# Optimization experiments

Measured on AMD Instinct MI355X. Metric: run time of the kernel, lower is better.

Reference implementation:

```python
import jax, jax.numpy as jnp
import numpy as np

B, N, D = 64, 256, 64          # datasets, samples per dataset, feature dim per variable (indim/2)
H, H2, OUT = 128, 64, 3        # hdlayers, hdlayers//2, outdim
REG, SIGMA, ALPHA = 1.0, 1.0, 2
BN_EPS = 1e-5


def _linear(k, fan_in, fan_out):
    kw, kb = jax.random.split(k)
    lim = 1.0 / np.sqrt(fan_in)
    w = jax.random.uniform(kw, (fan_in, fan_out), jnp.float32, -lim, lim)
    b = jax.random.uniform(kb, (fan_out,), jnp.float32, -lim, lim)
    return w, b


def setup_inputs() -> dict:
    key = jax.random.key(0)
    ks = jax.random.split(key, 10)
    w11_1, b11_1 = _linear(ks[2], D, H2)
    w11_2, b11_2 = _linear(ks[3], H2, H2)
    w12_1, b12_1 = _linear(ks[4], 2 * H2, H)
    w12_2, b12_2 = _linear(ks[5], H, H2)
    wc1, bc1 = _linear(ks[6], H2, OUT)
    w2, b2 = _linear(ks[7], OUT + 2, H2)
    wc2, bc2 = _linear(ks[8], H2, OUT)
    return {
        'x': jax.random.normal(ks[0], (B, N, D), jnp.float32),
        'y': jax.random.normal(ks[1], (B, N, D), jnp.float32),
        'w11_1': w11_1, 'b11_1': b11_1, 'w11_2': w11_2, 'b11_2': b11_2,
        'w12_1': w12_1, 'b12_1': b12_1, 'w12_2': w12_2, 'b12_2': b12_2,
        'wc1': wc1, 'bc1': bc1,
        'bn_gamma': jnp.ones((OUT + 2,), jnp.float32),
        'bn_beta': jnp.zeros((OUT + 2,), jnp.float32),
        'w2': w2, 'b2': b2, 'wc2': wc2, 'bc2': bc2,
    }


def _fro_normalize(t):
    # divide each [N, D] slice by its Frobenius norm
    return t / jnp.linalg.norm(t, axis=(1, 2), keepdims=True)


def _linear_regressor(x, y, reg):
    b, n, d = x.shape
    X = jnp.concatenate([jnp.ones((b, n, 1), x.dtype), x], axis=2)  # [B,N,d+1]
    P1 = jnp.einsum('bni,bnj->bij', X, X)                           # X^T X
    ridge = reg * jnp.eye(d + 1, dtype=x.dtype).at[0, 0].set(0.0)   # G^T G
    P2 = jnp.linalg.inv(P1 + ridge[None])
    P4 = X @ (P2 @ (jnp.swapaxes(X, 1, 2) @ y))
    loss = jnp.sum((y - P4) ** 2, axis=(1, 2))
    return loss, P4


def _gauss_kernel(x):
    # x: [B, N, F] -> [B, N, N]
    xn = jnp.sum(x * x, axis=-1)
    dist = xn[:, :, None] + xn[:, None, :] - 2.0 * jnp.einsum('bnd,bmd->bnm', x, x)
    return jnp.exp(-dist / SIGMA)


def _renyi_from_kernel(k):
    tr = jnp.trace(k, axis1=1, axis2=2)
    k = k / tr[:, None, None]
    ev = jnp.abs(jnp.linalg.eigvalsh(k))          # batched symeig eigenvalues
    return (1.0 / (1 - ALPHA)) * jnp.log2(jnp.sum(ev ** ALPHA, axis=-1))


def _renyi_mi(a, b):
    # batched normalized Renyi mutual information, a/b: [B, N, F]
    ka, kb = _gauss_kernel(a), _gauss_kernel(b)
    Hx = _renyi_from_kernel(ka)
    Hy = _renyi_from_kernel(kb)
    Hxy = _renyi_from_kernel(ka * kb)
    return (Hx + Hy - Hxy) / jnp.maximum(Hx, Hy)


def reference(x, y, w11_1, b11_1, w11_2, b11_2, w12_1, b12_1, w12_2, b12_2,
              wc1, bc1, bn_gamma, bn_beta, w2, b2, wc2, bc2):
    mlp11 = lambda t: jnp.maximum(t @ w11_1 + b11_1, 0.0) @ w11_2 + b11_2
    out_x = mlp11(x)                                  # [B,N,H2]
    out_y = mlp11(y)

    out_c = jnp.concatenate([out_x, out_y], axis=2)   # [B,N,2*H2]
    out_c = jnp.maximum(out_c @ w12_1 + b12_1, 0.0)
    out_c = jnp.maximum(out_c @ w12_2 + b12_2, 0.0)
    out_c = out_c.mean(axis=1)                        # [B,H2]
    out_c = out_c @ wc1 + bc1                         # [B,OUT]
    prob1 = jax.nn.softmax(out_c, axis=1)

    out_xn = _fro_normalize(out_x)
    out_yn = _fro_normalize(out_y)
    xx = _fro_normalize(x)
    yy = _fro_normalize(y)

    rx, px = _linear_regressor(out_xn, yy, REG)       # predict y from f(x)
    ry, py = _linear_regressor(out_yn, xx, REG)       # predict x from f(y)

    ex = _renyi_mi(yy - px, x)                        # [B]
    ey = _renyi_mi(xx - py, y)

    rxy = jnp.stack([ex, ey], axis=1)                 # [B,2]
    in_c = jnp.concatenate([out_c, rxy], axis=1)      # [B,OUT+2]
    mu = in_c.mean(axis=0)
    var = in_c.var(axis=0)                            # biased, as in torch BN training
    in_c = (in_c - mu) / jnp.sqrt(var + BN_EPS) * bn_gamma + bn_beta
    in_c = jnp.maximum(in_c @ w2 + b2, 0.0)
    out_c_f = in_c @ wc2 + bc2
    prob2 = jax.nn.softmax(out_c_f, axis=1)

    return (out_c, rx, ry, ex, ey, out_c_f, prob1, prob2)
```

## Files before the change

### kernel.cpp

```cpp
#include <hip/hip_runtime.h>
#include <math.h>

#define NB 64
#define NS 256
#define ND 64
#define NH2 64
#define NH 128
#define GSTRIDE 8448
#define WSTRIDE 4224


#define F4E(v_, e_) ((e_)==0?(v_).x:((e_)==1?(v_).y:((e_)==2?(v_).z:(v_).w)))

typedef __attribute__((ext_vector_type(8))) short bf16x8;
typedef __attribute__((ext_vector_type(4))) float f32x4;

__device__ __forceinline__ unsigned short f2bf(float f){
    union { float f; unsigned int u; } v; v.f = f;
    unsigned int r = v.u + 0x7fffu + ((v.u >> 16) & 1u);
    return (unsigned short)(r >> 16);
}
__device__ __forceinline__ float bf2f(unsigned short h){
    union { unsigned int u; float f; } v; v.u = ((unsigned int)h) << 16;
    return v.f;
}
__device__ __forceinline__ void sw2(unsigned short* ph, unsigned short* pl, int idx, float f){
    unsigned short h = f2bf(f);
    ph[idx] = h;
    pl[idx] = f2bf(f - bf2f(h));
}
__device__ __forceinline__ void sw2x2(unsigned short* ph, unsigned short* pl, int idx, float f0, float f1){
    unsigned short h0 = f2bf(f0), h1 = f2bf(f1);
    ushort2 hh; hh.x = h0; hh.y = h1;
    *(ushort2*)(ph + idx) = hh;
    ushort2 ll; ll.x = f2bf(f0 - bf2f(h0)); ll.y = f2bf(f1 - bf2f(h1));
    *(ushort2*)(pl + idx) = ll;
}

#define LD8(P_, row_, kb_) (*(const bf16x8*)((const char*)(P_) + (size_t)(row_)*144 + (kb_)))

__device__ __forceinline__ f32x4 mm64(
    const unsigned short* Ah, const unsigned short* Al,
    const unsigned short* Bh, const unsigned short* Bl,
    int ar, int br, int lrow, int lkb, f32x4 acc)
{
    const int ra = ar + lrow, rb = br + lrow;
    bf16x8 ah0 = LD8(Ah, ra, lkb), ah1 = LD8(Ah, ra, lkb+64);
    bf16x8 al0 = LD8(Al, ra, lkb), al1 = LD8(Al, ra, lkb+64);
    bf16x8 bh0 = LD8(Bh, rb, lkb), bh1 = LD8(Bh, rb, lkb+64);
    bf16x8 bl0 = LD8(Bl, rb, lkb), bl1 = LD8(Bl, rb, lkb+64);
    acc = __builtin_amdgcn_mfma_f32_16x16x32_bf16(ah0, bh0, acc, 0,0,0);
    acc = __builtin_amdgcn_mfma_f32_16x16x32_bf16(ah1, bh1, acc, 0,0,0);
    acc = __builtin_amdgcn_mfma_f32_16x16x32_bf16(ah0, bl0, acc, 0,0,0);
    acc = __builtin_amdgcn_mfma_f32_16x16x32_bf16(ah1, bl1, acc, 0,0,0);
    acc = __builtin_amdgcn_mfma_f32_16x16x32_bf16(al0, bh0, acc, 0,0,0);
    acc = __builtin_amdgcn_mfma_f32_16x16x32_bf16(al1, bh1, acc, 0,0,0);
    return acc;
}

__global__ __launch_bounds__(256) void k1_fused(
    const float* __restrict__ x, const float* __restrict__ y,
    const float* __restrict__ w11_1, const float* __restrict__ b11_1,
    const float* __restrict__ w11_2, const float* __restrict__ b11_2,
    const float* __restrict__ w12_1, const float* __restrict__ b12_1,
    const float* __restrict__ w12_2, const float* __restrict__ b12_2,
    float* __restrict__ out_x, float* __restrict__ out_y,
    float* __restrict__ mean_part)
{
    const int b = blockIdx.x >> 2, tile = blockIdx.x & 3;
    const int t = threadIdx.x;
    const int lane = t & 63, wv = t >> 6;
    const int lrow = lane & 15;
    const int lkb  = (lane >> 4) * 16;
    const int row0g = b*NS + tile*64;

    __shared__ unsigned short XYh[9216], XYl[9216];
    __shared__ unsigned short W1h[4608], W1l[4608];
    __shared__ unsigned short W2h[4608], W2l[4608];
    __shared__ unsigned short Hh [9216], Hl [9216];
    __shared__ unsigned short Oh [9216], Ol [9216];
    __shared__ float msum[4*68];

    #pragma unroll
    for (int u=0;u<8;u++){
        int id = t + 256*u;
        int r = id>>4, c0 = (id&15)*4;
        const float* src = (r < 64) ? (x + ((size_t)(row0g + r))*ND)
                                    : (y + ((size_t)(row0g + r - 64))*ND);
        float4 v = *(const float4*)(src + c0);
        sw2x2(XYh, XYl, r*72 + c0,   v.x, v.y);
        sw2x2(XYh, XYl, r*72 + c0+2, v.z, v.w);
    }
    #pragma unroll
    for (int u=0;u<2;u++){
        int id = t + 256*u;
        int rp = id>>4, c0 = (id&15)*4;
        float4 a0 = *(const float4*)(w11_1 + (size_t)(2*rp  )*64 + c0);
        float4 a1 = *(const float4*)(w11_1 + (size_t)(2*rp+1)*64 + c0);
        float4 b0 = *(const float4*)(w11_2 + (size_t)(2*rp  )*64 + c0);
        float4 b1 = *(const float4*)(w11_2 + (size_t)(2*rp+1)*64 + c0);
        #pragma unroll
        for (int i2=0;i2<4;i2++){
            sw2x2(W1h, W1l, (c0+i2)*72 + 2*rp, F4E(a0,i2), F4E(a1,i2));
            sw2x2(W2h, W2l, (c0+i2)*72 + 2*rp, F4E(b0,i2), F4E(b1,i2));
        }
    }
    __syncthreads();

    #pragma unroll
    for (int it=0; it<2; it++){
        const int ar = 32*wv + 16*it;
        #pragma unroll
        for (int jt=0; jt<4; jt++){
            float bb = b11_1[jt*16 + lrow];
            f32x4 acc = {bb,bb,bb,bb};
            acc = mm64(XYh, XYl, W1h, W1l, ar, jt*16, lrow, lkb, acc);
            #pragma unroll
            for (int e=0;e<4;e++){
                int row = ar + (lane>>4)*4 + e;
                int col = jt*16 + lrow;
                sw2(Hh, Hl, row*72 + col, fmaxf(acc[e], 0.f));
            }
        }
    }
    __syncthreads();

    #pragma unroll
    for (int u=0;u<4;u++){
        int id = t + 256*u;
        int krp = id>>5, c0 = (id&31)*4;
        float4 v0 = *(const float4*)(w12_1 + (size_t)(2*krp  )*NH + c0);
        float4 v1 = *(const float4*)(w12_1 + (size_t)(2*krp+1)*NH + c0);
        #pragma unroll
        for (int i2=0;i2<4;i2++)
            sw2x2(XYh, XYl, (c0+i2)*72 + 2*krp, F4E(v0,i2), F4E(v1,i2));
    }
    #pragma unroll
    for (int it=0; it<2; it++){
        const int ar = 32*wv + 16*it;
        #pragma unroll
        for (int jt=0; jt<4; jt++){
            float bb = b11_2[jt*16 + lrow];
            f32x4 acc = {bb,bb,bb,bb};
            acc = mm64(Hh, Hl, W2h, W2l, ar, jt*16, lrow, lkb, acc);
            #pragma unroll
            for (int e=0;e<4;e++){
                int row = ar + (lane>>4)*4 + e;
                int col = jt*16 + lrow;
                float v = acc[e];
                sw2(Oh, Ol, row*72 + col, v);
                float* dst = (row < 64) ? out_x : out_y;
                dst[((size_t)(row0g + (row & 63)))*NH2 + col] = v;
            }
        }
    }
    __syncthreads();

    f32x4 acc3[8];
    #pragma unroll
    for (int jt=0; jt<8; jt++){
        float bb = b12_1[jt*16 + lrow];
        f32x4 v = {bb,bb,bb,bb};
        acc3[jt] = v;
    }
    #pragma unroll
    for (int jt=0; jt<8; jt++)
        acc3[jt] = mm64(Oh, Ol, XYh, XYl, 16*wv, jt*16, lrow, lkb, acc3[jt]);
    __syncthreads();

    #pragma unroll
    for (int u=0;u<4;u++){
        int id = t + 256*u;
        int krp = id>>5, c0 = (id&31)*4;
        float4 v0 = *(const float4*)(w12_1 + (size_t)(64+2*krp  )*NH + c0);
        float4 v1 = *(const float4*)(w12_1 + (size_t)(64+2*krp+1)*NH + c0);
        #pragma unroll
        for (int i2=0;i2<4;i2++)
            sw2x2(XYh, XYl, (c0+i2)*72 + 2*krp, F4E(v0,i2), F4E(v1,i2));
    }
    #pragma unroll
    for (int u=0;u<2;u++){
        int id = t + 256*u;
        int krp = id>>4, c0 = (id&15)*4;
        float4 h0a = *(const float4*)(w12_2 + (size_t)(2*krp  )*NH2 + c0);
        float4 h0b = *(const float4*)(w12_2 + (size_t)(2*krp+1)*NH2 + c0);
        float4 h1a = *(const float4*)(w12_2 + (size_t)(64+2*krp  )*NH2 + c0);
        float4 h1b = *(const float4*)(w12_2 + (size_t)(64+2*krp+1)*NH2 + c0);
        #pragma unroll
        for (int i2=0;i2<4;i2++){
            sw2x2(W2h, W2l, (c0+i2)*72 + 2*krp, F4E(h0a,i2), F4E(h0b,i2));
            sw2x2(W1h, W1l, (c0+i2)*72 + 2*krp, F4E(h1a,i2), F4E(h1b,i2));
        }
    }
    __syncthreads();

    #pragma unroll
    for (int jt=0; jt<8; jt++)
        acc3[jt] = mm64(Oh, Ol, XYh, XYl, 64 + 16*wv, jt*16, lrow, lkb, acc3[jt]);
    #pragma unroll
    for (int jt=0; jt<8; jt++){
        #pragma unroll
        for (int e=0;e<4;e++){
            int row = 16*wv + (lane>>4)*4 + e;
            int col = jt*16 + lrow;
            float v = fmaxf(acc3[jt][e], 0.f);
            int idx = (col < 64) ? (row*72 + col) : ((64+row)*72 + (col-64));
            sw2(Hh, Hl, idx, v);
        }
    }
    __syncthreads();

    {
        f32x4 acc2[4];
        #pragma unroll
        for (int jt=0; jt<4; jt++){
            float bb = b12_2[jt*16 + lrow];
            f32x4 v = {bb,bb,bb,bb};
            acc2[jt] = v;
        }
        #pragma unroll
        for (int jt=0; jt<4; jt++){
            acc2[jt] = mm64(Hh, Hl, W2h, W2l, 16*wv,      jt*16, lrow, lkb, acc2[jt]);
            acc2[jt] = mm64(Hh, Hl, W1h, W1l, 64 + 16*wv, jt*16, lrow, lkb, acc2[jt]);
        }
        #pragma unroll
        for (int jt=0; jt<4; jt++){
            float s = fmaxf(acc2[jt][0],0.f) + fmaxf(acc2[jt][1],0.f)
                    + fmaxf(acc2[jt][2],0.f) + fmaxf(acc2[jt][3],0.f);
            s += __shfl_down(s, 32);
            s += __shfl_down(s, 16);
            if (lane < 16) msum[wv*68 + jt*16 + lane] = s;
        }
    }
    __syncthreads();
    if (t < 64){
        float ss = msum[t] + msum[68+t] + msum[2*68+t] + msum[3*68+t];
        mean_part[((size_t)(b*4+tile))*64 + t] = ss;
    }
}

__global__ __launch_bounds__(256) void k2a_build(
    const float* __restrict__ fx, const float* __restrict__ fy,
    const float* __restrict__ x, const float* __restrict__ y,
    float* __restrict__ gram)
{
    const int blk = blockIdx.x;
    const int kh = blk & 1, side = (blk>>1)&1, b = blk>>2;
    const float* feat = side ? fy : fx;
    const float* targ = side ? x : y;
    float* g = gram + (size_t)blk*GSTRIDE;
    const int t = threadIdx.x;
    const int ig2 = t & 15, jg2 = t >> 4;
    const int i0 = ig2*4, j0 = jg2*4;
    __shared__ float Zt[64*68], Tt[64*68];
    __shared__ float red[4];

    float accA[4][4], accR[4][4];
    #pragma unroll
    for (int u=0;u<4;u++)
        #pragma unroll
        for (int v=0;v<4;v++){ accA[u][v]=0.f; accR[u][v]=0.f; }
    float szp=0.f, stp=0.f, tsqp=0.f;
    const int cc_ = t & 63, rq = t >> 6;

    for (int sub=0; sub<2; sub++){
        if (sub) __syncthreads();
        const int r0g = b*NS + kh*128 + sub*64;
        #pragma unroll
        for (int u=0;u<4;u++){
            int id = t + 256*u; int r = id>>4, c4 = (id&15)*4;
            *(float4*)(Zt + r*68 + c4) = *(const float4*)(feat + ((size_t)(r0g+r))*NH2 + c4);
            *(float4*)(Tt + r*68 + c4) = *(const float4*)(targ + ((size_t)(r0g+r))*ND + c4);
        }
        __syncthreads();
        #pragma unroll
        for (int ch=0; ch<16; ch++){
            const int r0 = ch*4;
            float4 zi[4], zj[4], tj[4];
            #pragma unroll
            for (int c=0;c<4;c++){
                zi[c] = *(const float4*)(Zt + (r0+c)*68 + i0);
                zj[c] = *(const float4*)(Zt + (r0+c)*68 + j0);
                tj[c] = *(const float4*)(Tt + (r0+c)*68 + j0);
            }
            #pragma unroll
            for (int c=0;c<4;c++){
                #pragma unroll
                for (int u=0;u<4;u++){
                    const float zv = F4E(zi[c], u);
                    const float4 a4 = zj[c], r4 = tj[c];
                    accA[u][0] += zv*a4.x; accA[u][1] += zv*a4.y;
                    accA[u][2] += zv*a4.z; accA[u][3] += zv*a4.w;
                    accR[u][0] += zv*r4.x; accR[u][1] += zv*r4.y;
                    accR[u][2] += zv*r4.z; accR[u][3] += zv*r4.w;
                }
            }
        }
        #pragma unroll
        for (int rr=0; rr<16; rr++){
            int r = rq*16 + rr;
            szp += Zt[r*68 + cc_];
            float tv = Tt[r*68 + cc_];
            stp += tv; tsqp += tv*tv;
        }
    }
    #pragma unroll
    for (int u=0;u<4;u++){
        *(float4*)(g + (i0+u)*64 + j0) = make_float4(accA[u][0],accA[u][1],accA[u][2],accA[u][3]);
        *(float4*)(g + 4096 + (i0+u)*64 + j0) = make_float4(accR[u][0],accR[u][1],accR[u][2],accR[u][3]);
    }
    __syncthreads();
    Zt[rq*68 + cc_] = szp;
    Tt[rq*68 + cc_] = stp;
    float tq = tsqp;
    #pragma unroll
    for (int off=32; off; off>>=1) tq += __shfl_down(tq, off);
    if ((t&63)==0) red[t>>6] = tq;
    __syncthreads();
    if (t < 64){
        g[8192+t] = Zt[t] + Zt[68+t] + Zt[2*68+t] + Zt[3*68+t];
        g[8256+t] = Tt[t] + Tt[68+t] + Tt[2*68+t] + Tt[3*68+t];
    }
    if (t==0) g[8320] = red[0]+red[1]+red[2]+red[3];
}

__global__ __launch_bounds__(256) void k2b_solve(
    const float* __restrict__ gram, float* __restrict__ wbuf)
{
    const int bs = blockIdx.x;
    const float* g0 = gram + (size_t)(bs*2+0)*GSTRIDE;
    const float* g1 = gram + (size_t)(bs*2+1)*GSTRIDE;
    float* wb = wbuf + (size_t)bs*WSTRIDE;
    const int t = threadIdx.x;
    const int lane = t & 63, wv = t >> 6;
    const int lrow = lane & 15;
    const int lkb  = (lane >> 4) * 16;

    __shared__ float Rf[64*68];
    __shared__ float Wf[64*68];
    __shared__ unsigned short Eh[4608], El[4608];
    __shared__ unsigned short Wth[2][4608], Wtl[2][4608];
    __shared__ float szs[64], sts[64];
    __shared__ float sc[8];

    #pragma unroll
    for (int u=0;u<16;u++){
        int id = t + 256*u; int r = id>>6, c = id&63;
        Wf[r*68+c] = g0[id] + g1[id];
        Rf[r*68+c] = g0[4096+id] + g1[4096+id];
    }
    if (t<64){ szs[t] = g0[8192+t]+g1[8192+t]; sts[t] = g0[8256+t]+g1[8256+t]; }
    if (t==0) sc[1] = g0[8320]+g1[8320];
    __syncthreads();
    if (t<64){
        float dg = Wf[t*68+t];
        #pragma unroll
        for (int off=32; off; off>>=1) dg += __shfl_down(dg, off);
        if (t==0){ sc[0] = 1.0f/sqrtf(dg); sc[1] = 1.0f/sqrtf(sc[1]); }
    }
    __syncthreads();
    const float zinv = sc[0], tinv = sc[1];
    const float z2 = zinv*zinv, zt = zinv*tinv, inv256 = 1.0f/256.0f;
    const float i23 = 2.0f/3.0f;
    const int i = t>>2, qd = t&3;
    {
        const float szi = szs[i];
        #pragma unroll
        for (int q=0;q<4;q++){
            const int j = qd*16 + q*4;
            float4 a4 = *(const float4*)(Wf + i*68 + j);
            float4 sj = *(const float4*)(szs + j);
            float v0 = z2*(a4.x - szi*sj.x*inv256);
            float v1 = z2*(a4.y - szi*sj.y*inv256);
            float v2 = z2*(a4.z - szi*sj.z*inv256);
            float v3 = z2*(a4.w - szi*sj.w*inv256);
            if (i == j)   v0 += 1.f;
            else if (i == j+1) v1 += 1.f;
            else if (i == j+2) v2 += 1.f;
            else if (i == j+3) v3 += 1.f;
            float e0 = v0*i23 - ((i==j  ) ? 1.f : 0.f);
            float e1 = v1*i23 - ((i==j+1) ? 1.f : 0.f);
            float e2 = v2*i23 - ((i==j+2) ? 1.f : 0.f);
            float e3 = v3*i23 - ((i==j+3) ? 1.f : 0.f);
            sw2x2(Eh, El, i*72 + j,   e0, e1);
            sw2x2(Eh, El, i*72 + j+2, e2, e3);
            float4 rv = *(float4*)(Rf + i*68 + j);
            float4 t4 = *(const float4*)(sts + j);
            float r0 = zt*(rv.x - szi*t4.x*inv256)*i23;
            float r1 = zt*(rv.y - szi*t4.y*inv256)*i23;
            float r2 = zt*(rv.z - szi*t4.z*inv256)*i23;
            float r3 = zt*(rv.w - szi*t4.w*inv256)*i23;
            *(float4*)(Rf + i*68 + j) = make_float4(r0,r1,r2,r3);
            sw2(Wth[0], Wtl[0], (j  )*72 + i, r0);
            sw2(Wth[0], Wtl[0], (j+1)*72 + i, r1);
            sw2(Wth[0], Wtl[0], (j+2)*72 + i, r2);
            sw2(Wth[0], Wtl[0], (j+3)*72 + i, r3);
        }
    }
    __syncthreads();

    int cur = 0;
    for (int n=0; n<12; n++){
        f32x4 acc[4];
        #pragma unroll
        for (int jt=0; jt<4; jt++){
            f32x4 zz = {0.f,0.f,0.f,0.f};
            acc[jt] = mm64(Eh, El, Wth[cur], Wtl[cur], 16*wv, jt*16, lrow, lkb, zz);
        }
        const int gi0 = 16*wv + (lane>>4)*4;
        #pragma unroll
        for (int jt=0; jt<4; jt++){
            const int gj = jt*16 + lrow;
            float w0 = Rf[(gi0  )*68 + gj] - acc[jt][0];
            float w1 = Rf[(gi0+1)*68 + gj] - acc[jt][1];
            float w2 = Rf[(gi0+2)*68 + gj] - acc[jt][2];
            float w3 = Rf[(gi0+3)*68 + gj] - acc[jt][3];
            sw2x2(Wth[cur^1], Wtl[cur^1], gj*72 + gi0,   w0, w1);
            sw2x2(Wth[cur^1], Wtl[cur^1], gj*72 + gi0+2, w2, w3);
            if (n == 11){
                Wf[(gi0  )*68 + gj] = w0;  wb[(gi0  )*64 + gj] = w0;
                Wf[(gi0+1)*68 + gj] = w1;  wb[(gi0+1)*64 + gj] = w1;
                Wf[(gi0+2)*68 + gj] = w2;  wb[(gi0+2)*64 + gj] = w2;
                Wf[(gi0+3)*68 + gj] = w3;  wb[(gi0+3)*64 + gj] = w3;
            }
        }
        cur ^= 1;
        __syncthreads();
    }

    if (t < 64){
        float s = 0.f;
        for (int i2=0; i2<64; i2++) s += szs[i2]*Wf[i2*68 + t];
        wb[4096+t] = (tinv*sts[t] - zinv*s) * inv256;
    }
    if (t==0){ wb[4160] = zinv; wb[4161] = tinv; }
}

__global__ __launch_bounds__(256) void kRG(
    const float* __restrict__ fx, const float* __restrict__ fy,
    const float* __restrict__ x, const float* __restrict__ y,
    const float* __restrict__ wbuf,
    float* __restrict__ part3, float* __restrict__ dout)
{
    const int blk = blockIdx.x;
    const int jh = blk & 1;
    const int b = (blk >> 1) & (NB-1);
    const int side = (blk >> 1) >> 6;
    const float* feat = side ? fy : fx;
    const float* targ = side ? x : y;
    const float* bmat = side ? y : x;
    const float* wb = wbuf + (size_t)(b*2+side)*WSTRIDE;
    const int t = threadIdx.x;
    const int lane = t & 63, wv = t >> 6;
    const int lrow = lane & 15, lkb = (lane>>4)*16;

    __shared__ unsigned short resA[256*72];
    __shared__ unsigned short tgB [256*72];
    __shared__ unsigned short Zh[2*4608], Zl[2*4608];
    __shared__ unsigned short Wth[4608], Wtl[4608];
    __shared__ float c0s[64];
    __shared__ float nAs[256], nBs[256];
    __shared__ float red[4][3];
    __shared__ float lred[4];

    #pragma unroll
    for (int u=0;u<4;u++){
        int id = t + 256*u;
        int k = id>>4, c0 = (id&15)*4;
        float4 v = *(const float4*)(wb + (size_t)k*64 + c0);
        sw2(Wth, Wtl, (c0+0)*72 + k, v.x);
        sw2(Wth, Wtl, (c0+1)*72 + k, v.y);
        sw2(Wth, Wtl, (c0+2)*72 + k, v.z);
        sw2(Wth, Wtl, (c0+3)*72 + k, v.w);
    }
    if (t<64) c0s[t] = wb[4096+t];
    const float zinv = wb[4160], tinv = wb[4161];
    #pragma unroll
    for (int u=0;u<16;u++){
        int id = t + 256*u;
        int r = id>>4, c0 = (id&15)*4;
        float4 v = *(const float4*)(bmat + ((size_t)(b*NS+r))*ND + c0);
        ushort4 h;
        h.x=f2bf(v.x); h.y=f2bf(v.y); h.z=f2bf(v.z); h.w=f2bf(v.w);
        *(ushort4*)(tgB + r*72 + c0) = h;
    }
    #pragma unroll
    for (int u=0;u<4;u++){
        int id = t + 256*u;
        int r = id>>4, c0 = (id&15)*4;
        float4 v = *(const float4*)(feat + ((size_t)(b*NS + r))*NH2 + c0);
        sw2x2(Zh, Zl, r*72+c0,   v.x, v.y);
        sw2x2(Zh, Zl, r*72+c0+2, v.z, v.w);
    }
    __syncthreads();

    float lacc = 0.f;
    for (int c=0; c<4; c++){
        if (c < 3){
            unsigned short* zh = Zh + ((c+1)&1)*4608;
            unsigned short* zl = Zl + ((c+1)&1)*4608;
            #pragma unroll
            for (int u=0;u<4;u++){
                int id = t + 256*u;
                int r = id>>4, c0 = (id&15)*4;
                float4 v = *(const float4*)(feat + ((size_t)(b*NS + (c+1)*64 + r))*NH2 + c0);
                sw2x2(zh, zl, r*72+c0,   v.x, v.y);
                sw2x2(zh, zl, r*72+c0+2, v.z, v.w);
            }
        }
        const unsigned short* zh = Zh + (c&1)*4608;
        const unsigned short* zl = Zl + (c&1)*4608;
        f32x4 acc[4];
        #pragma unroll
        for (int jt=0; jt<4; jt++){
            f32x4 zz = {0.f,0.f,0.f,0.f};
            acc[jt] = mm64(zh, zl, Wth, Wtl, 16*wv, jt*16, lrow, lkb, zz);
        }
        const int r0 = 16*wv + (lane>>4)*4;
        #pragma unroll
        for (int jt=0; jt<4; jt++){
            const int gj = jt*16 + lrow;
            const float cc = c0s[gj];
            #pragma unroll
            for (int e=0;e<4;e++){
                const int grow = c*64 + r0 + e;
                float q = targ[((size_t)(b*NS+grow))*ND + gj];
                float rr = tinv*q - zinv*acc[jt][e] - cc;
                lacc += rr*rr;
                resA[grow*72 + gj] = f2bf(rr);
            }
        }
        __syncthreads();
    }

    {
        float l = lacc;
        #pragma unroll
        for (int off=32; off; off>>=1) l += __shfl_down(l, off);
        if (lane==0) lred[wv] = l;
    }
    {
        float sa=0.f, sb=0.f;
        #pragma unroll
        for (int j8=0;j8<8;j8++){
            bf16x8 va = *(const bf16x8*)((const char*)resA + (size_t)t*144 + j8*16);
            bf16x8 vb = *(const bf16x8*)((const char*)tgB  + (size_t)t*144 + j8*16);
            #pragma unroll
            for (int e2=0;e2<8;e2++){
                float fa = bf2f((unsigned short)va[e2]);
                float fb = bf2f((unsigned short)vb[e2]);
                sa += fa*fa; sb += fb*fb;
            }
        }
        nAs[t] = sa; nBs[t] = sb;
    }
    __syncthreads();
    if (t==0 && jh==0)
        dout[(side?256:192)+b] = lred[0]+lred[1]+lred[2]+lred[3];

    const char* pA = (const char*)resA;
    const char* pB = (const char*)tgB;
    const f32x4 zero4 = {0.f, 0.f, 0.f, 0.f};
    const float CEXP = -2.8853900817779268f;

    float Sa=0.f, Sb=0.f, Sab=0.f;
    #pragma unroll
    for (int it=0; it<4; it++){
        const int i0 = wv*64 + it*16;
        const int arow = i0 + lrow;
        bf16x8 aA0 = *(const bf16x8*)(pA + arow*144 + lkb);
        bf16x8 aA1 = *(const bf16x8*)(pA + arow*144 + lkb + 64);
        bf16x8 aB0 = *(const bf16x8*)(pB + arow*144 + lkb);
        bf16x8 aB1 = *(const bf16x8*)(pB + arow*144 + lkb + 64);
        float nAi[4], nBi[4];
        #pragma unroll
        for (int e=0;e<4;e++){
            int gi = i0 + (lane>>4)*4 + e;
            nAi[e] = nAs[gi]; nBi[e] = nBs[gi];
        }
        #pragma unroll
        for (int jt=0; jt<8; jt++){
            const int j0 = jh*128 + jt*16;
            const int brow = j0 + lrow;
            bf16x8 bA0 = *(const bf16x8*)(pA + brow*144 + lkb);
            bf16x8 bA1 = *(const bf16x8*)(pA + brow*144 + lkb + 64);
            bf16x8 bB0 = *(const bf16x8*)(pB + brow*144 + lkb);
            bf16x8 bB1 = *(const bf16x8*)(pB + brow*144 + lkb + 64);
            f32x4 cA = __builtin_amdgcn_mfma_f32_16x16x32_bf16(aA0, bA0, zero4, 0, 0, 0);
            cA = __builtin_amdgcn_mfma_f32_16x16x32_bf16(aA1, bA1, cA, 0, 0, 0);
            f32x4 cB = __builtin_amdgcn_mfma_f32_16x16x32_bf16(aB0, bB0, zero4, 0, 0, 0);
            cB = __builtin_amdgcn_mfma_f32_16x16x32_bf16(aB1, bB1, cB, 0, 0, 0);
            const int gj = j0 + lrow;
            const float nAj = nAs[gj], nBj = nBs[gj];
            #pragma unroll
            for (int e=0;e<4;e++){
                const int gi = i0 + (lane>>4)*4 + e;
                const float dda = (gi==gj) ? 0.f : (nAi[e] + nAj - 2.f*cA[e]);
                const float ddb = (gi==gj) ? 0.f : (nBi[e] + nBj - 2.f*cB[e]);
                const float ka2 = exp2f(CEXP*dda);
                const float kb2 = exp2f(CEXP*ddb);
                Sa += ka2; Sb += kb2; Sab += ka2*kb2;
            }
        }
    }
    #pragma unroll
    for (int off=32; off; off>>=1){
        Sa += __shfl_down(Sa,off); Sb += __shfl_down(Sb,off); Sab += __shfl_down(Sab,off);
    }
    if (lane==0){ red[wv][0]=Sa; red[wv][1]=Sb; red[wv][2]=Sab; }
    __syncthreads();
    if (t==0){
        float* o = part3 + (size_t)blk*3;
        o[0] = red[0][0]+red[1][0]+red[2][0]+red[3][0];
        o[1] = red[0][1]+red[1][1]+red[2][1]+red[3][1];
        o[2] = red[0][2]+red[1][2]+red[2][2]+red[3][2];
    }
}

__global__ __launch_bounds__(64) void k4_final(
    const float* __restrict__ mean_part, const float* __restrict__ part3,
    const float* __restrict__ wc1, const float* __restrict__ bc1,
    const float* __restrict__ bn_gamma, const float* __restrict__ bn_beta,
    const float* __restrict__ w2, const float* __restrict__ b2,
    const float* __restrict__ wc2, const float* __restrict__ bc2,
    float* __restrict__ dout)
{
    const int t = threadIdx.x;
    __shared__ float ic[64][5];
    __shared__ float mu[5], iv[5];

    float o0 = bc1[0], o1 = bc1[1], o2 = bc1[2];
    for (int c=0;c<64;c++){
        float mv = mean_part[(t*4+0)*64+c] + mean_part[(t*4+1)*64+c]
                 + mean_part[(t*4+2)*64+c] + mean_part[(t*4+3)*64+c];
        mv *= (1.0f/256.0f);
        o0 += mv*wc1[c*3+0]; o1 += mv*wc1[c*3+1]; o2 += mv*wc1[c*3+2];
    }
    dout[t*3+0]=o0; dout[t*3+1]=o1; dout[t*3+2]=o2;
    {
        float m = fmaxf(o0,fmaxf(o1,o2));
        float e0=__expf(o0-m), e1=__expf(o1-m), e2=__expf(o2-m);
        float inv = 1.f/(e0+e1+e2);
        dout[640+t*3+0]=e0*inv; dout[640+t*3+1]=e1*inv; dout[640+t*3+2]=e2*inv;
    }
    float exy[2];
    #pragma unroll
    for (int side=0; side<2; side++){
        const float* pp = part3 + (size_t)((side*NB + t)*2)*3;
        float Sa = pp[0]+pp[3];
        float Sb = pp[1]+pp[4];
        float Sab= pp[2]+pp[5];
        float Hx  = 16.f - log2f(Sa);
        float Hy  = 16.f - log2f(Sb);
        float Hxy = 16.f - log2f(Sab);
        float mi = (Hx + Hy - Hxy) / fmaxf(Hx, Hy);
        dout[(side?384:320)+t] = mi;
        exy[side] = mi;
    }
    ic[t][0]=o0; ic[t][1]=o1; ic[t][2]=o2; ic[t][3]=exy[0]; ic[t][4]=exy[1];
    __syncthreads();
    if (t<5){
        float m=0.f;
        for (int bb=0;bb<64;bb++) m += ic[bb][t];
        m *= (1.f/64.f);
        float v=0.f;
        for (int bb=0;bb<64;bb++){ float d=ic[bb][t]-m; v+=d*d; }
        v *= (1.f/64.f);
        mu[t]=m; iv[t]=1.f/sqrtf(v+1e-5f);
    }
    __syncthreads();
    float vn[5];
    #pragma unroll
    for (int c=0;c<5;c++) vn[c] = (ic[t][c]-mu[c])*iv[c]*bn_gamma[c]+bn_beta[c];
    float q0=bc2[0], q1=bc2[1], q2=bc2[2];
    for (int j=0;j<64;j++){
        float hh = b2[j];
        #pragma unroll
        for (int c=0;c<5;c++) hh += vn[c]*w2[c*64+j];
        hh = fmaxf(hh,0.f);
        q0 += hh*wc2[j*3+0]; q1 += hh*wc2[j*3+1]; q2 += hh*wc2[j*3+2];
    }
    dout[448+t*3+0]=q0; dout[448+t*3+1]=q1; dout[448+t*3+2]=q2;
    float m = fmaxf(q0,fmaxf(q1,q2));
    float e0=__expf(q0-m), e1=__expf(q1-m), e2=__expf(q2-m);
    float inv=1.f/(e0+e1+e2);
    dout[832+t*3+0]=e0*inv; dout[832+t*3+1]=e1*inv; dout[832+t*3+2]=e2*inv;
}

extern "C" void kernel_launch(void* const* d_in, const int* in_sizes, int n_in,
                              void* d_out, int out_size, void* d_ws, size_t ws_size,
                              hipStream_t stream)
{
    const float* x     = (const float*)d_in[0];
    const float* y     = (const float*)d_in[1];
    const float* w11_1 = (const float*)d_in[2];
    const float* b11_1 = (const float*)d_in[3];
    const float* w11_2 = (const float*)d_in[4];
    const float* b11_2 = (const float*)d_in[5];
    const float* w12_1 = (const float*)d_in[6];
    const float* b12_1 = (const float*)d_in[7];
    const float* w12_2 = (const float*)d_in[8];
    const float* b12_2 = (const float*)d_in[9];
    const float* wc1   = (const float*)d_in[10];
    const float* bc1   = (const float*)d_in[11];
    const float* bn_g  = (const float*)d_in[12];
    const float* bn_b  = (const float*)d_in[13];
    const float* w2    = (const float*)d_in[14];
    const float* b2    = (const float*)d_in[15];
    const float* wc2   = (const float*)d_in[16];
    const float* bc2   = (const float*)d_in[17];

    float* ws   = (float*)d_ws;
    float* dout = (float*)d_out;
    float* out_x = ws;
    float* out_y = ws + 1048576;
    float* mean_part = ws + 4259840;
    float* part3 = mean_part + 16384;
    float* gram  = ws + 4280320;
    float* wbuf  = gram + 2162688;

    hipLaunchKernelGGL(k1_fused, dim3(NB*4), dim3(256), 0, stream,
        x,y,w11_1,b11_1,w11_2,b11_2,w12_1,b12_1,w12_2,b12_2,
        out_x,out_y,mean_part);
    hipLaunchKernelGGL(k2a_build, dim3(NB*4), dim3(256), 0, stream,
        out_x,out_y,x,y,gram);
    hipLaunchKernelGGL(k2b_solve, dim3(2*NB), dim3(256), 0, stream,
        gram,wbuf);
    hipLaunchKernelGGL(kRG, dim3(NB*2*2), dim3(256), 0, stream,
        out_x,out_y,x,y,wbuf,part3,dout);
    hipLaunchKernelGGL(k4_final, dim3(1), dim3(64), 0, stream,
        mean_part,part3,wc1,bc1,bn_g,bn_b,w2,b2,wc2,bc2,dout);
}
```

Measured before the change: 85.25 us.

## Fuse Gram build into solve kernel with MFMA and widen k1 to 512 threads

Merges the Gram-matrix build and the solve kernels into one, so the partial Gram matrices no longer go through global memory and one launch is saved. The Gram products are now computed with split-bf16 MFMA on mean-centred features instead of scalar FMAs with a later mean correction. k1_fused is widened to 512 threads with 8 waves sharing the work. The fused kernel has only 128 blocks, each reading a full dataset, which lowers parallelism and adds a second pass over the inputs for the column sums.

```diff
diff --git a/kernel.cpp b/kernel.cpp
--- a/kernel.cpp
+++ b/kernel.cpp
@@ -6,7 +6,6 @@
 #define ND 64
 #define NH2 64
 #define NH 128
-#define GSTRIDE 8448
 #define WSTRIDE 4224
 
 
@@ -58,7 +57,7 @@
     return acc;
 }
 
-__global__ __launch_bounds__(256) void k1_fused(
+__global__ __launch_bounds__(512) void k1_fused(
     const float* __restrict__ x, const float* __restrict__ y,
     const float* __restrict__ w11_1, const float* __restrict__ b11_1,
     const float* __restrict__ w11_2, const float* __restrict__ b11_2,
@@ -79,11 +78,11 @@
     __shared__ unsigned short W2h[4608], W2l[4608];
     __shared__ unsigned short Hh [9216], Hl [9216];
     __shared__ unsigned short Oh [9216], Ol [9216];
-    __shared__ float msum[4*68];
-
-    #pragma unroll
-    for (int u=0;u<8;u++){
-        int id = t + 256*u;
+    __shared__ float msum[8*68];
+
+    #pragma unroll
+    for (int u=0;u<4;u++){
+        int id = t + 512*u;
         int r = id>>4, c0 = (id&15)*4;
         const float* src = (r < 64) ? (x + ((size_t)(row0g + r))*ND)
                                     : (y + ((size_t)(row0g + r - 64))*ND);
@@ -91,10 +90,8 @@
         sw2x2(XYh, XYl, r*72 + c0,   v.x, v.y);
         sw2x2(XYh, XYl, r*72 + c0+2, v.z, v.w);
     }
-    #pragma unroll
-    for (int u=0;u<2;u++){
-        int id = t + 256*u;
-        int rp = id>>4, c0 = (id&15)*4;
+    {
+        int rp = t>>4, c0 = (t&15)*4;
         float4 a0 = *(const float4*)(w11_1 + (size_t)(2*rp  )*64 + c0);
         float4 a1 = *(const float4*)(w11_1 + (size_t)(2*rp+1)*64 + c0);
         float4 b0 = *(const float4*)(w11_2 + (size_t)(2*rp  )*64 + c0);
@@ -107,9 +104,8 @@
     }
     __syncthreads();
 
-    #pragma unroll
-    for (int it=0; it<2; it++){
-        const int ar = 32*wv + 16*it;
+    {
+        const int ar = 16*wv;
         #pragma unroll
         for (int jt=0; jt<4; jt++){
             float bb = b11_1[jt*16 + lrow];
@@ -126,8 +122,8 @@
     __syncthreads();
 
     #pragma unroll
-    for (int u=0;u<4;u++){
-        int id = t + 256*u;
+    for (int u=0;u<2;u++){
+        int id = t + 512*u;
         int krp = id>>5, c0 = (id&31)*4;
         float4 v0 = *(const float4*)(w12_1 + (size_t)(2*krp  )*NH + c0);
         float4 v1 = *(const float4*)(w12_1 + (size_t)(2*krp+1)*NH + c0);
@@ -135,9 +131,8 @@
         for (int i2=0;i2<4;i2++)
             sw2x2(XYh, XYl, (c0+i2)*72 + 2*krp, F4E(v0,i2), F4E(v1,i2));
     }
-    #pragma unroll
-    for (int it=0; it<2; it++){
-        const int ar = 32*wv + 16*it;
+    {
+        const int ar = 16*wv;
         #pragma unroll
         for (int jt=0; jt<4; jt++){
             float bb = b11_2[jt*16 + lrow];
@@ -156,21 +151,22 @@
     }
     __syncthreads();
 
-    f32x4 acc3[8];
-    #pragma unroll
-    for (int jt=0; jt<8; jt++){
-        float bb = b12_1[jt*16 + lrow];
+    const int rt = wv & 3, cq = wv >> 2;
+    f32x4 acc3[4];
+    #pragma unroll
+    for (int q=0; q<4; q++){
+        float bb = b12_1[(4*cq+q)*16 + lrow];
         f32x4 v = {bb,bb,bb,bb};
-        acc3[jt] = v;
-    }
-    #pragma unroll
-    for (int jt=0; jt<8; jt++)
-        acc3[jt] = mm64(Oh, Ol, XYh, XYl, 16*wv, jt*16, lrow, lkb, acc3[jt]);
-    __syncthreads();
-
-    #pragma unroll
-    for (int u=0;u<4;u++){
-        int id = t + 256*u;
+        acc3[q] = v;
+    }
+    #pragma unroll
+    for (int q=0; q<4; q++)
+        acc3[q] = mm64(Oh, Ol, XYh, XYl, 16*rt, 16*(4*cq+q), lrow, lkb, acc3[q]);
+    __syncthreads();
+
+    #pragma unroll
+    for (int u=0;u<2;u++){
+        int id = t + 512*u;
         int krp = id>>5, c0 = (id&31)*4;
         float4 v0 = *(const float4*)(w12_1 + (size_t)(64+2*krp  )*NH + c0);
         float4 v1 = *(const float4*)(w12_1 + (size_t)(64+2*krp+1)*NH + c0);
@@ -178,10 +174,8 @@
         for (int i2=0;i2<4;i2++)
             sw2x2(XYh, XYl, (c0+i2)*72 + 2*krp, F4E(v0,i2), F4E(v1,i2));
     }
-    #pragma unroll
-    for (int u=0;u<2;u++){
-        int id = t + 256*u;
-        int krp = id>>4, c0 = (id&15)*4;
+    {
+        int krp = t>>4, c0 = (t&15)*4;
         float4 h0a = *(const float4*)(w12_2 + (size_t)(2*krp  )*NH2 + c0);
         float4 h0b = *(const float4*)(w12_2 + (size_t)(2*krp+1)*NH2 + c0);
         float4 h1a = *(const float4*)(w12_2 + (size_t)(64+2*krp  )*NH2 + c0);
@@ -195,15 +189,15 @@
     __syncthreads();
 
     #pragma unroll
-    for (int jt=0; jt<8; jt++)
-        acc3[jt] = mm64(Oh, Ol, XYh, XYl, 64 + 16*wv, jt*16, lrow, lkb, acc3[jt]);
-    #pragma unroll
-    for (int jt=0; jt<8; jt++){
+    for (int q=0; q<4; q++)
+        acc3[q] = mm64(Oh, Ol, XYh, XYl, 64 + 16*rt, 16*(4*cq+q), lrow, lkb, acc3[q]);
+    #pragma unroll
+    for (int q=0; q<4; q++){
         #pragma unroll
         for (int e=0;e<4;e++){
-            int row = 16*wv + (lane>>4)*4 + e;
-            int col = jt*16 + lrow;
-            float v = fmaxf(acc3[jt][e], 0.f);
+            int row = 16*rt + (lane>>4)*4 + e;
+            int col = 16*(4*cq+q) + lrow;
+            float v = fmaxf(acc3[q][e], 0.f);
             int idx = (col < 64) ? (row*72 + col) : ((64+row)*72 + (col-64));
             sw2(Hh, Hl, idx, v);
         }
@@ -211,185 +205,171 @@
     __syncthreads();
 
     {
-        f32x4 acc2[4];
-        #pragma unroll
-        for (int jt=0; jt<4; jt++){
-            float bb = b12_2[jt*16 + lrow];
+        f32x4 acc2[2];
+        #pragma unroll
+        for (int q=0; q<2; q++){
+            const int jc = 2*cq + q;
+            float bb = b12_2[jc*16 + lrow];
             f32x4 v = {bb,bb,bb,bb};
-            acc2[jt] = v;
-        }
-        #pragma unroll
-        for (int jt=0; jt<4; jt++){
-            acc2[jt] = mm64(Hh, Hl, W2h, W2l, 16*wv,      jt*16, lrow, lkb, acc2[jt]);
-            acc2[jt] = mm64(Hh, Hl, W1h, W1l, 64 + 16*wv, jt*16, lrow, lkb, acc2[jt]);
-        }
-        #pragma unroll
-        for (int jt=0; jt<4; jt++){
-            float s = fmaxf(acc2[jt][0],0.f) + fmaxf(acc2[jt][1],0.f)
-                    + fmaxf(acc2[jt][2],0.f) + fmaxf(acc2[jt][3],0.f);
+            acc2[q] = v;
+            acc2[q] = mm64(Hh, Hl, W2h, W2l, 16*rt,      16*jc, lrow, lkb, acc2[q]);
+            acc2[q] = mm64(Hh, Hl, W1h, W1l, 64 + 16*rt, 16*jc, lrow, lkb, acc2[q]);
+        }
+        #pragma unroll
+        for (int q=0; q<2; q++){
+            const int jc = 2*cq + q;
+            float s = fmaxf(acc2[q][0],0.f) + fmaxf(acc2[q][1],0.f)
+                    + fmaxf(acc2[q][2],0.f) + fmaxf(acc2[q][3],0.f);
             s += __shfl_down(s, 32);
             s += __shfl_down(s, 16);
-            if (lane < 16) msum[wv*68 + jt*16 + lane] = s;
+            if (lane < 16) msum[wv*68 + jc*16 + lane] = s;
         }
     }
     __syncthreads();
     if (t < 64){
-        float ss = msum[t] + msum[68+t] + msum[2*68+t] + msum[3*68+t];
+        const int w0 = (t>>5)*4;
+        float ss = msum[(w0+0)*68 + t] + msum[(w0+1)*68 + t]
+                 + msum[(w0+2)*68 + t] + msum[(w0+3)*68 + t];
         mean_part[((size_t)(b*4+tile))*64 + t] = ss;
     }
 }
 
-__global__ __launch_bounds__(256) void k2a_build(
+__global__ __launch_bounds__(256) void k2ab(
     const float* __restrict__ fx, const float* __restrict__ fy,
     const float* __restrict__ x, const float* __restrict__ y,
-    float* __restrict__ gram)
+    float* __restrict__ wbuf)
 {
-    const int blk = blockIdx.x;
-    const int kh = blk & 1, side = (blk>>1)&1, b = blk>>2;
+    const int bs = blockIdx.x;
+    const int side = bs & 1, b = bs >> 1;
     const float* feat = side ? fy : fx;
     const float* targ = side ? x : y;
-    float* g = gram + (size_t)blk*GSTRIDE;
-    const int t = threadIdx.x;
-    const int ig2 = t & 15, jg2 = t >> 4;
-    const int i0 = ig2*4, j0 = jg2*4;
-    __shared__ float Zt[64*68], Tt[64*68];
-    __shared__ float red[4];
-
-    float accA[4][4], accR[4][4];
-    #pragma unroll
-    for (int u=0;u<4;u++)
-        #pragma unroll
-        for (int v=0;v<4;v++){ accA[u][v]=0.f; accR[u][v]=0.f; }
-    float szp=0.f, stp=0.f, tsqp=0.f;
-    const int cc_ = t & 63, rq = t >> 6;
-
-    for (int sub=0; sub<2; sub++){
-        if (sub) __syncthreads();
-        const int r0g = b*NS + kh*128 + sub*64;
-        #pragma unroll
-        for (int u=0;u<4;u++){
-            int id = t + 256*u; int r = id>>4, c4 = (id&15)*4;
-            *(float4*)(Zt + r*68 + c4) = *(const float4*)(feat + ((size_t)(r0g+r))*NH2 + c4);
-            *(float4*)(Tt + r*68 + c4) = *(const float4*)(targ + ((size_t)(r0g+r))*ND + c4);
-        }
-        __syncthreads();
-        #pragma unroll
-        for (int ch=0; ch<16; ch++){
-            const int r0 = ch*4;
-            float4 zi[4], zj[4], tj[4];
-            #pragma unroll
-            for (int c=0;c<4;c++){
-                zi[c] = *(const float4*)(Zt + (r0+c)*68 + i0);
-                zj[c] = *(const float4*)(Zt + (r0+c)*68 + j0);
-                tj[c] = *(const float4*)(Tt + (r0+c)*68 + j0);
-            }
-            #pragma unroll
-            for (int c=0;c<4;c++){
-                #pragma unroll
-                for (int u=0;u<4;u++){
-                    const float zv = F4E(zi[c], u);
-                    const float4 a4 = zj[c], r4 = tj[c];
-                    accA[u][0] += zv*a4.x; accA[u][1] += zv*a4.y;
-                    accA[u][2] += zv*a4.z; accA[u][3] += zv*a4.w;
-                    accR[u][0] += zv*r4.x; accR[u][1] += zv*r4.y;
-                    accR[u][2] += zv*r4.z; accR[u][3] += zv*r4.w;
-                }
-            }
-        }
-        #pragma unroll
-        for (int rr=0; rr<16; rr++){
-            int r = rq*16 + rr;
-            szp += Zt[r*68 + cc_];
-            float tv = Tt[r*68 + cc_];
-            stp += tv; tsqp += tv*tv;
-        }
-    }
-    #pragma unroll
-    for (int u=0;u<4;u++){
-        *(float4*)(g + (i0+u)*64 + j0) = make_float4(accA[u][0],accA[u][1],accA[u][2],accA[u][3]);
-        *(float4*)(g + 4096 + (i0+u)*64 + j0) = make_float4(accR[u][0],accR[u][1],accR[u][2],accR[u][3]);
-    }
-    __syncthreads();
-    Zt[rq*68 + cc_] = szp;
-    Tt[rq*68 + cc_] = stp;
-    float tq = tsqp;
-    #pragma unroll
-    for (int off=32; off; off>>=1) tq += __shfl_down(tq, off);
-    if ((t&63)==0) red[t>>6] = tq;
-    __syncthreads();
-    if (t < 64){
-        g[8192+t] = Zt[t] + Zt[68+t] + Zt[2*68+t] + Zt[3*68+t];
-        g[8256+t] = Tt[t] + Tt[68+t] + Tt[2*68+t] + Tt[3*68+t];
-    }
-    if (t==0) g[8320] = red[0]+red[1]+red[2]+red[3];
-}
-
-__global__ __launch_bounds__(256) void k2b_solve(
-    const float* __restrict__ gram, float* __restrict__ wbuf)
-{
-    const int bs = blockIdx.x;
-    const float* g0 = gram + (size_t)(bs*2+0)*GSTRIDE;
-    const float* g1 = gram + (size_t)(bs*2+1)*GSTRIDE;
     float* wb = wbuf + (size_t)bs*WSTRIDE;
     const int t = threadIdx.x;
     const int lane = t & 63, wv = t >> 6;
     const int lrow = lane & 15;
     const int lkb  = (lane >> 4) * 16;
-
+    const float inv256 = 1.0f/256.0f;
+
+    __shared__ float Wf[64*68];
     __shared__ float Rf[64*68];
-    __shared__ float Wf[64*68];
+    __shared__ unsigned short Zh[4608], Zl[4608], Th[4608], Tl[4608];
     __shared__ unsigned short Eh[4608], El[4608];
     __shared__ unsigned short Wth[2][4608], Wtl[2][4608];
+    __shared__ float cspA[16*68], cspB[16*68];
     __shared__ float szs[64], sts[64];
-    __shared__ float sc[8];
-
-    #pragma unroll
-    for (int u=0;u<16;u++){
-        int id = t + 256*u; int r = id>>6, c = id&63;
-        Wf[r*68+c] = g0[id] + g1[id];
-        Rf[r*68+c] = g0[4096+id] + g1[4096+id];
-    }
-    if (t<64){ szs[t] = g0[8192+t]+g1[8192+t]; sts[t] = g0[8256+t]+g1[8256+t]; }
-    if (t==0) sc[1] = g0[8320]+g1[8320];
+    __shared__ float sc[8], red4[4];
+
+    {
+        float szp0=0.f,szp1=0.f,szp2=0.f,szp3=0.f;
+        float stp0=0.f,stp1=0.f,stp2=0.f,stp3=0.f;
+        float tsq=0.f;
+        for (int c=0;c<4;c++){
+            #pragma unroll
+            for (int u=0;u<4;u++){
+                int id = t + 256*u;
+                int r = id>>4, c0 = (id&15)*4;
+                float4 v = *(const float4*)(feat + ((size_t)(b*NS + c*64 + r))*NH2 + c0);
+                float4 w = *(const float4*)(targ + ((size_t)(b*NS + c*64 + r))*ND + c0);
+                szp0+=v.x; szp1+=v.y; szp2+=v.z; szp3+=v.w;
+                stp0+=w.x; stp1+=w.y; stp2+=w.z; stp3+=w.w;
+                tsq += w.x*w.x + w.y*w.y + w.z*w.z + w.w*w.w;
+            }
+        }
+        const int g2 = t>>4, c0 = (t&15)*4;
+        cspA[g2*68 + c0+0] = szp0; cspA[g2*68 + c0+1] = szp1;
+        cspA[g2*68 + c0+2] = szp2; cspA[g2*68 + c0+3] = szp3;
+        cspB[g2*68 + c0+0] = stp0; cspB[g2*68 + c0+1] = stp1;
+        cspB[g2*68 + c0+2] = stp2; cspB[g2*68 + c0+3] = stp3;
+        float tq = tsq;
+        #pragma unroll
+        for (int off=32; off; off>>=1) tq += __shfl_down(tq, off);
+        if (lane==0) red4[wv] = tq;
+    }
+    __syncthreads();
+    if (t < 64){
+        float sa=0.f, sb=0.f;
+        #pragma unroll
+        for (int g2=0; g2<16; g2++){ sa += cspA[g2*68+t]; sb += cspB[g2*68+t]; }
+        szs[t] = sa; sts[t] = sb;
+        float s2 = sa*sa;
+        #pragma unroll
+        for (int off=32; off; off>>=1) s2 += __shfl_down(s2, off);
+        if (t==0) sc[2] = s2;
+    }
+    if (t==0) sc[1] = red4[0]+red4[1]+red4[2]+red4[3];
+    __syncthreads();
+
+    f32x4 accA[4], accR[4];
+    #pragma unroll
+    for (int jt=0;jt<4;jt++){
+        f32x4 z = {0.f,0.f,0.f,0.f};
+        accA[jt]=z; accR[jt]=z;
+    }
+    for (int c=0;c<4;c++){
+        if (c) __syncthreads();
+        #pragma unroll
+        for (int u=0;u<4;u++){
+            int id = t + 256*u;
+            int r = id>>4, c0 = (id&15)*4;
+            float4 v = *(const float4*)(feat + ((size_t)(b*NS + c*64 + r))*NH2 + c0);
+            float4 w = *(const float4*)(targ + ((size_t)(b*NS + c*64 + r))*ND + c0);
+            v.x -= szs[c0+0]*inv256; v.y -= szs[c0+1]*inv256;
+            v.z -= szs[c0+2]*inv256; v.w -= szs[c0+3]*inv256;
+            sw2(Zh,Zl,(c0+0)*72+r, v.x); sw2(Zh,Zl,(c0+1)*72+r, v.y);
+            sw2(Zh,Zl,(c0+2)*72+r, v.z); sw2(Zh,Zl,(c0+3)*72+r, v.w);
+            sw2(Th,Tl,(c0+0)*72+r, w.x); sw2(Th,Tl,(c0+1)*72+r, w.y);
+            sw2(Th,Tl,(c0+2)*72+r, w.z); sw2(Th,Tl,(c0+3)*72+r, w.w);
+        }
+        __syncthreads();
+        #pragma unroll
+        for (int jt=0;jt<4;jt++){
+            accA[jt] = mm64(Zh,Zl,Zh,Zl, 16*wv, 16*jt, lrow, lkb, accA[jt]);
+            accR[jt] = mm64(Zh,Zl,Th,Tl, 16*wv, 16*jt, lrow, lkb, accR[jt]);
+        }
+    }
+    {
+        const int gi0 = 16*wv + (lane>>4)*4;
+        #pragma unroll
+        for (int jt=0;jt<4;jt++){
+            #pragma unroll
+            for (int e=0;e<4;e++){
+                Wf[(gi0+e)*68 + 16*jt + lrow] = accA[jt][e];
+                Rf[(gi0+e)*68 + 16*jt + lrow] = accR[jt][e];
+            }
+        }
+    }
     __syncthreads();
     if (t<64){
         float dg = Wf[t*68+t];
         #pragma unroll
         for (int off=32; off; off>>=1) dg += __shfl_down(dg, off);
-        if (t==0){ sc[0] = 1.0f/sqrtf(dg); sc[1] = 1.0f/sqrtf(sc[1]); }
+        if (t==0){
+            float zn2 = dg + sc[2]*inv256;
+            sc[0] = 1.0f/sqrtf(zn2);
+            sc[1] = 1.0f/sqrtf(sc[1]);
+        }
     }
     __syncthreads();
     const float zinv = sc[0], tinv = sc[1];
-    const float z2 = zinv*zinv, zt = zinv*tinv, inv256 = 1.0f/256.0f;
-    const float i23 = 2.0f/3.0f;
+    const float z2 = zinv*zinv, zt = zinv*tinv;
+    const float i23 = 2.0f/3.0f, i13 = 1.0f/3.0f;
     const int i = t>>2, qd = t&3;
     {
-        const float szi = szs[i];
         #pragma unroll
         for (int q=0;q<4;q++){
             const int j = qd*16 + q*4;
             float4 a4 = *(const float4*)(Wf + i*68 + j);
-            float4 sj = *(const float4*)(szs + j);
-            float v0 = z2*(a4.x - szi*sj.x*inv256);
-            float v1 = z2*(a4.y - szi*sj.y*inv256);
-            float v2 = z2*(a4.z - szi*sj.z*inv256);
-            float v3 = z2*(a4.w - szi*sj.w*inv256);
-            if (i == j)   v0 += 1.f;
-            else if (i == j+1) v1 += 1.f;
-            else if (i == j+2) v2 += 1.f;
-            else if (i == j+3) v3 += 1.f;
-            float e0 = v0*i23 - ((i==j  ) ? 1.f : 0.f);
-            float e1 = v1*i23 - ((i==j+1) ? 1.f : 0.f);
-            float e2 = v2*i23 - ((i==j+2) ? 1.f : 0.f);
-            float e3 = v3*i23 - ((i==j+3) ? 1.f : 0.f);
+            float e0 = i23*z2*a4.x - ((i==j  ) ? i13 : 0.f);
+            float e1 = i23*z2*a4.y - ((i==j+1) ? i13 : 0.f);
+            float e2 = i23*z2*a4.z - ((i==j+2) ? i13 : 0.f);
+            float e3 = i23*z2*a4.w - ((i==j+3) ? i13 : 0.f);
             sw2x2(Eh, El, i*72 + j,   e0, e1);
             sw2x2(Eh, El, i*72 + j+2, e2, e3);
             float4 rv = *(float4*)(Rf + i*68 + j);
-            float4 t4 = *(const float4*)(sts + j);
-            float r0 = zt*(rv.x - szi*t4.x*inv256)*i23;
-            float r1 = zt*(rv.y - szi*t4.y*inv256)*i23;
-            float r2 = zt*(rv.z - szi*t4.z*inv256)*i23;
-            float r3 = zt*(rv.w - szi*t4.w*inv256)*i23;
+            float r0 = i23*zt*rv.x;
+            float r1 = i23*zt*rv.y;
+            float r2 = i23*zt*rv.z;
+            float r3 = i23*zt*rv.w;
             *(float4*)(Rf + i*68 + j) = make_float4(r0,r1,r2,r3);
             sw2(Wth[0], Wtl[0], (j  )*72 + i, r0);
             sw2(Wth[0], Wtl[0], (j+1)*72 + i, r1);
@@ -714,18 +694,15 @@
     float* dout = (float*)d_out;
     float* out_x = ws;
     float* out_y = ws + 1048576;
-    float* mean_part = ws + 4259840;
+    float* mean_part = ws + 2097152;
     float* part3 = mean_part + 16384;
-    float* gram  = ws + 4280320;
-    float* wbuf  = gram + 2162688;
-
-    hipLaunchKernelGGL(k1_fused, dim3(NB*4), dim3(256), 0, stream,
+    float* wbuf  = part3 + 3840;
+
+    hipLaunchKernelGGL(k1_fused, dim3(NB*4), dim3(512), 0, stream,
         x,y,w11_1,b11_1,w11_2,b11_2,w12_1,b12_1,w12_2,b12_2,
         out_x,out_y,mean_part);
-    hipLaunchKernelGGL(k2a_build, dim3(NB*4), dim3(256), 0, stream,
-        out_x,out_y,x,y,gram);
-    hipLaunchKernelGGL(k2b_solve, dim3(2*NB), dim3(256), 0, stream,
-        gram,wbuf);
+    hipLaunchKernelGGL(k2ab, dim3(2*NB), dim3(256), 0, stream,
+        out_x,out_y,x,y,wbuf);
     hipLaunchKernelGGL(kRG, dim3(NB*2*2), dim3(256), 0, stream,
         out_x,out_y,x,y,wbuf,part3,dout);
     hipLaunchKernelGGL(k4_final, dim3(1), dim3(64), 0, stream,
```

New measurement: 79.80 us. 1.07x faster.
